# Kernel tuning notes

Measured on AMD Instinct MI355X. Metric: run time of the kernel, lower is better.

Reference implementation:

```python
import jax, jax.numpy as jnp
import numpy as np

UP_TIME = 1440.0
UP_DIST = 40.0
LOC_CNT = 100000
LOC_LEN = 131072
H = 256


def setup_inputs() -> dict:
    key = jax.random.key(0)
    ks = jax.random.split(key, 12)
    stdv = 1.0 / np.sqrt(H)
    u = lambda k, shape: jax.random.uniform(k, shape, jnp.float32, -stdv, stdv)
    return {
        "td_upper": jax.random.uniform(ks[0], (LOC_LEN,), jnp.float32),
        "td_lower": jax.random.uniform(ks[1], (LOC_LEN,), jnp.float32),
        "ld_upper": jax.random.uniform(ks[2], (LOC_LEN,), jnp.float32),
        "ld_lower": jax.random.uniform(ks[3], (LOC_LEN,), jnp.float32),
        "loc": jax.random.randint(ks[4], (LOC_LEN,), 0, LOC_CNT, jnp.int32),
        "hx": jax.random.normal(ks[5], (H, 1), jnp.float32),
        "weight_ih": u(ks[6], (H, H)),
        "weight_th_upper": u(ks[7], (H, H)),
        "weight_th_lower": u(ks[8], (H, H)),
        "weight_sh_upper": u(ks[9], (H, H)),
        "weight_sh_lower": u(ks[10], (H, H)),
        "location_weight": u(ks[11], (LOC_CNT, H)),
    }


def reference(td_upper, td_lower, ld_upper, ld_lower, loc, hx,
              weight_ih, weight_th_upper, weight_th_lower,
              weight_sh_upper, weight_sh_lower, location_weight):
    tu = jnp.clip(td_upper, 0.0, UP_TIME)
    tl = jnp.clip(td_lower, 0.0, UP_TIME)
    lu = jnp.clip(ld_upper, 0.0, UP_DIST)
    ll = jnp.clip(ld_lower, 0.0, UP_DIST)

    e = location_weight[loc]  # [L, H] gathered POI embeddings
    # Ttd[i] @ e[i] = (tu[i]*W_tu@e[i] + tl[i]*W_tl@e[i]) / (tu[i]+tl[i])
    a = jnp.einsum('hk,lk->lh', weight_th_upper, e)
    b = jnp.einsum('hk,lk->lh', weight_th_lower, e)
    t = (tu[:, None] * a + tl[:, None] * b) / (tu + tl)[:, None]  # [L, H]
    # Sld[i] @ t[i]
    c = jnp.einsum('hk,lk->lh', weight_sh_upper, t)
    d = jnp.einsum('hk,lk->lh', weight_sh_lower, t)
    s = (lu[:, None] * c + ll[:, None] * d) / (lu + ll)[:, None]  # [L, H]

    loc_vec = jnp.sum(s, axis=0)[:, None]  # [H, 1]
    usr_vec = weight_ih @ hx               # [H, 1]
    return jax.nn.sigmoid(loc_vec + usr_vec)
```

## Files before the change

### kernel.cpp

```cpp
#include <hip/hip_runtime.h>
#include <math.h>

#define H 256
#define TILE 256

__global__ __launch_bounds__(256) void strnn_gather(
    const float* __restrict__ td_u, const float* __restrict__ td_l,
    const float* __restrict__ ld_u, const float* __restrict__ ld_l,
    const int* __restrict__ loc, const float* __restrict__ table,
    float* __restrict__ v, int L)
{
    __shared__ float4 s_w[TILE];
    __shared__ int    s_loc[TILE];
    __shared__ float  s_red[4][4][H];
    const int t    = threadIdx.x;
    const int wave = t >> 6;
    const int lane = t & 63;

    float4 a0 = {0,0,0,0}, a1 = {0,0,0,0}, a2 = {0,0,0,0}, a3 = {0,0,0,0};

    for (int base = blockIdx.x * TILE; base < L; base += gridDim.x * TILE) {
        const int l = base + t;
        const bool ok = (l < L);
        float tu = ok ? fminf(fmaxf(td_u[l], 0.f), 1440.f) : 1.f;
        float tl = ok ? fminf(fmaxf(td_l[l], 0.f), 1440.f) : 1.f;
        float lu = ok ? fminf(fmaxf(ld_u[l], 0.f), 40.f)   : 1.f;
        float ll = ok ? fminf(fmaxf(ld_l[l], 0.f), 40.f)   : 1.f;
        float al = tu / (tu + tl);
        float be = lu / (lu + ll);
        float w0 = be * al, w1 = be * (1.f - al);
        float w2 = (1.f - be) * al, w3 = (1.f - be) * (1.f - al);
        if (!ok) { w0 = w1 = w2 = w3 = 0.f; }
        s_w[t]   = make_float4(w0, w1, w2, w3);
        s_loc[t] = ok ? loc[l] : 0;
        __syncthreads();

        const int r0 = wave * 64;
        #pragma unroll 2
        for (int j = 0; j < 64; j += 8) {
            const float4* addr[8];
            #pragma unroll
            for (int u = 0; u < 8; ++u)
                addr[u] = (const float4*)(table + (size_t)s_loc[r0 + j + u] * H + 4 * lane);
            float4 w[8], e[8];
            #pragma unroll
            for (int u = 0; u < 8; ++u)
                e[u] = *addr[u];
            #pragma unroll
            for (int u = 0; u < 8; ++u)
                w[u] = s_w[r0 + j + u];
            #pragma unroll
            for (int u = 0; u < 8; ++u) {
                a0.x = fmaf(w[u].x, e[u].x, a0.x);
                a0.y = fmaf(w[u].x, e[u].y, a0.y);
                a0.z = fmaf(w[u].x, e[u].z, a0.z);
                a0.w = fmaf(w[u].x, e[u].w, a0.w);
                a1.x = fmaf(w[u].y, e[u].x, a1.x);
                a1.y = fmaf(w[u].y, e[u].y, a1.y);
                a1.z = fmaf(w[u].y, e[u].z, a1.z);
                a1.w = fmaf(w[u].y, e[u].w, a1.w);
                a2.x = fmaf(w[u].z, e[u].x, a2.x);
                a2.y = fmaf(w[u].z, e[u].y, a2.y);
                a2.z = fmaf(w[u].z, e[u].z, a2.z);
                a2.w = fmaf(w[u].z, e[u].w, a2.w);
                a3.x = fmaf(w[u].w, e[u].x, a3.x);
                a3.y = fmaf(w[u].w, e[u].y, a3.y);
                a3.z = fmaf(w[u].w, e[u].z, a3.z);
                a3.w = fmaf(w[u].w, e[u].w, a3.w);
            }
        }
        __syncthreads();
    }

    *(float4*)&s_red[wave][0][4 * lane] = a0;
    *(float4*)&s_red[wave][1][4 * lane] = a1;
    *(float4*)&s_red[wave][2][4 * lane] = a2;
    *(float4*)&s_red[wave][3][4 * lane] = a3;
    __syncthreads();
    #pragma unroll
    for (int c = 0; c < 4; ++c) {
        float s = s_red[0][c][t] + s_red[1][c][t] + s_red[2][c][t] + s_red[3][c][t];
        atomicAdd(&v[c * H + t], s);
    }
}

__global__ __launch_bounds__(256) void strnn_mid(
    const float* __restrict__ Wtu, const float* __restrict__ Wtl,
    const float* __restrict__ Wih, const float* __restrict__ hx,
    const float* __restrict__ v, float* __restrict__ pqu)
{
    const int wave = (blockIdx.x * blockDim.x + threadIdx.x) >> 6;
    const int lane = threadIdx.x & 63;
    const float* v1 = v;
    const float* v2 = v + H;
    const float* v3 = v + 2 * H;
    const float* v4 = v + 3 * H;

    float p = 0.f, q = 0.f, u = 0.f;
    #pragma unroll
    for (int i = 0; i < H; i += 64) {
        const int k = i + lane;
        const float wtu = Wtu[wave * H + k];
        const float wtl = Wtl[wave * H + k];
        p = fmaf(wtu, v1[k], fmaf(wtl, v2[k], p));
        q = fmaf(wtu, v3[k], fmaf(wtl, v4[k], q));
        u = fmaf(Wih[wave * H + k], hx[k], u);
    }
    #pragma unroll
    for (int off = 32; off > 0; off >>= 1) {
        p += __shfl_down(p, off, 64);
        q += __shfl_down(q, off, 64);
        u += __shfl_down(u, off, 64);
    }
    if (lane == 0) {
        pqu[wave]         = p;
        pqu[H + wave]     = q;
        pqu[2 * H + wave] = u;
    }
}

__global__ __launch_bounds__(256) void strnn_out(
    const float* __restrict__ Wsu, const float* __restrict__ Wsl,
    const float* __restrict__ pqu, float* __restrict__ out)
{
    const int wave = (blockIdx.x * blockDim.x + threadIdx.x) >> 6;
    const int lane = threadIdx.x & 63;
    const float* p = pqu;
    const float* q = pqu + H;
    const float* u = pqu + 2 * H;

    float s = 0.f;
    #pragma unroll
    for (int i = 0; i < H; i += 64) {
        const int k = i + lane;
        s = fmaf(Wsu[wave * H + k], p[k], fmaf(Wsl[wave * H + k], q[k], s));
    }
    #pragma unroll
    for (int off = 32; off > 0; off >>= 1)
        s += __shfl_down(s, off, 64);
    if (lane == 0)
        out[wave] = 1.f / (1.f + expf(-(s + u[wave])));
}

extern "C" void kernel_launch(void* const* d_in, const int* in_sizes, int n_in,
                              void* d_out, int out_size, void* d_ws, size_t ws_size,
                              hipStream_t stream) {
    const float* td_u  = (const float*)d_in[0];
    const float* td_l  = (const float*)d_in[1];
    const float* ld_u  = (const float*)d_in[2];
    const float* ld_l  = (const float*)d_in[3];
    const int*   loc   = (const int*)d_in[4];
    const float* hx    = (const float*)d_in[5];
    const float* Wih   = (const float*)d_in[6];
    const float* Wtu   = (const float*)d_in[7];
    const float* Wtl   = (const float*)d_in[8];
    const float* Wsu   = (const float*)d_in[9];
    const float* Wsl   = (const float*)d_in[10];
    const float* table = (const float*)d_in[11];
    const int L = in_sizes[0];

    float* v   = (float*)d_ws;
    float* pqu = v + 4 * H;

    hipMemsetAsync(v, 0, 4 * H * sizeof(float), stream);

    strnn_gather<<<512, 256, 0, stream>>>(td_u, td_l, ld_u, ld_l, loc, table, v, L);
    strnn_mid<<<64, 256, 0, stream>>>(Wtu, Wtl, Wih, hx, v, pqu);
    strnn_out<<<64, 256, 0, stream>>>(Wsu, Wsl, pqu, (float*)d_out);
}
```

Measured before the change: 183.7 us.

## Aggregate weights per location by scatter, then stream embedding table once

Each sequence element's four mixing weights are now atomically added into a per-location weight buffer. A second kernel then streams the embedding table row by row, reading only rows with nonzero weight, and accumulates the weighted sums. This swaps random 1KB-per-element gathers, including repeated rows, for a mostly sequential pass over the table. The cost is global float atomics, a larger workspace memset and an extra kernel launch.

New measurement: 208.7 us. 1.14x slower.

```diff
diff --git a/kernel.cpp b/kernel.cpp
--- a/kernel.cpp
+++ b/kernel.cpp
@@ -2,74 +2,76 @@
 #include <math.h>
 
 #define H 256
-#define TILE 256
 
-__global__ __launch_bounds__(256) void strnn_gather(
+__global__ __launch_bounds__(256) void strnn_scatter(
     const float* __restrict__ td_u, const float* __restrict__ td_l,
     const float* __restrict__ ld_u, const float* __restrict__ ld_l,
-    const int* __restrict__ loc, const float* __restrict__ table,
-    float* __restrict__ v, int L)
+    const int* __restrict__ loc, float* __restrict__ W, int L)
 {
-    __shared__ float4 s_w[TILE];
-    __shared__ int    s_loc[TILE];
-    __shared__ float  s_red[4][4][H];
+    int i = blockIdx.x * blockDim.x + threadIdx.x;
+    const int stride = gridDim.x * blockDim.x;
+    for (; i < L; i += stride) {
+        const float tu = fminf(fmaxf(td_u[i], 0.f), 1440.f);
+        const float tl = fminf(fmaxf(td_l[i], 0.f), 1440.f);
+        const float lu = fminf(fmaxf(ld_u[i], 0.f), 40.f);
+        const float ll = fminf(fmaxf(ld_l[i], 0.f), 40.f);
+        const float al = tu / (tu + tl);
+        const float be = lu / (lu + ll);
+        float* Wr = W + 4 * (size_t)loc[i];
+        atomicAdd(Wr + 0, be * al);
+        atomicAdd(Wr + 1, be * (1.f - al));
+        atomicAdd(Wr + 2, (1.f - be) * al);
+        atomicAdd(Wr + 3, (1.f - be) * (1.f - al));
+    }
+}
+
+__global__ __launch_bounds__(512) void strnn_accum(
+    const float* __restrict__ W, const float* __restrict__ table,
+    float* __restrict__ v, int R)
+{
+    __shared__ float s_red[8][4][H];
     const int t    = threadIdx.x;
     const int wave = t >> 6;
     const int lane = t & 63;
+    const int nwave = gridDim.x * 8;
 
     float4 a0 = {0,0,0,0}, a1 = {0,0,0,0}, a2 = {0,0,0,0}, a3 = {0,0,0,0};
 
-    for (int base = blockIdx.x * TILE; base < L; base += gridDim.x * TILE) {
-        const int l = base + t;
-        const bool ok = (l < L);
-        float tu = ok ? fminf(fmaxf(td_u[l], 0.f), 1440.f) : 1.f;
-        float tl = ok ? fminf(fmaxf(td_l[l], 0.f), 1440.f) : 1.f;
-        float lu = ok ? fminf(fmaxf(ld_u[l], 0.f), 40.f)   : 1.f;
-        float ll = ok ? fminf(fmaxf(ld_l[l], 0.f), 40.f)   : 1.f;
-        float al = tu / (tu + tl);
-        float be = lu / (lu + ll);
-        float w0 = be * al, w1 = be * (1.f - al);
-        float w2 = (1.f - be) * al, w3 = (1.f - be) * (1.f - al);
-        if (!ok) { w0 = w1 = w2 = w3 = 0.f; }
-        s_w[t]   = make_float4(w0, w1, w2, w3);
-        s_loc[t] = ok ? loc[l] : 0;
-        __syncthreads();
-
-        const int r0 = wave * 64;
-        #pragma unroll 2
-        for (int j = 0; j < 64; j += 8) {
-            const float4* addr[8];
-            #pragma unroll
-            for (int u = 0; u < 8; ++u)
-                addr[u] = (const float4*)(table + (size_t)s_loc[r0 + j + u] * H + 4 * lane);
-            float4 w[8], e[8];
-            #pragma unroll
-            for (int u = 0; u < 8; ++u)
-                e[u] = *addr[u];
-            #pragma unroll
-            for (int u = 0; u < 8; ++u)
-                w[u] = s_w[r0 + j + u];
-            #pragma unroll
-            for (int u = 0; u < 8; ++u) {
-                a0.x = fmaf(w[u].x, e[u].x, a0.x);
-                a0.y = fmaf(w[u].x, e[u].y, a0.y);
-                a0.z = fmaf(w[u].x, e[u].z, a0.z);
-                a0.w = fmaf(w[u].x, e[u].w, a0.w);
-                a1.x = fmaf(w[u].y, e[u].x, a1.x);
-                a1.y = fmaf(w[u].y, e[u].y, a1.y);
-                a1.z = fmaf(w[u].y, e[u].z, a1.z);
-                a1.w = fmaf(w[u].y, e[u].w, a1.w);
-                a2.x = fmaf(w[u].z, e[u].x, a2.x);
-                a2.y = fmaf(w[u].z, e[u].y, a2.y);
-                a2.z = fmaf(w[u].z, e[u].z, a2.z);
-                a2.w = fmaf(w[u].z, e[u].w, a2.w);
-                a3.x = fmaf(w[u].w, e[u].x, a3.x);
-                a3.y = fmaf(w[u].w, e[u].y, a3.y);
-                a3.z = fmaf(w[u].w, e[u].z, a3.z);
-                a3.w = fmaf(w[u].w, e[u].w, a3.w);
-            }
+    for (int r0 = (blockIdx.x * 8 + wave) * 8; r0 < R; r0 += nwave * 8) {
+        float4 wv[8], e[8];
+        #pragma unroll
+        for (int u = 0; u < 8; ++u) {
+            const int r = r0 + u;
+            wv[u] = (r < R) ? *(const float4*)(W + 4 * (size_t)r)
+                            : make_float4(0.f, 0.f, 0.f, 0.f);
         }
-        __syncthreads();
+        #pragma unroll
+        for (int u = 0; u < 8; ++u) {
+            e[u] = make_float4(0.f, 0.f, 0.f, 0.f);
+            const float4 w = wv[u];
+            if (w.x != 0.f || w.y != 0.f || w.z != 0.f || w.w != 0.f)
+                e[u] = *(const float4*)(table + (size_t)(r0 + u) * H + 4 * lane);
+        }
+        #pragma unroll
+        for (int u = 0; u < 8; ++u) {
+            const float4 w = wv[u];
+            a0.x = fmaf(w.x, e[u].x, a0.x);
+            a0.y = fmaf(w.x, e[u].y, a0.y);
+            a0.z = fmaf(w.x, e[u].z, a0.z);
+            a0.w = fmaf(w.x, e[u].w, a0.w);
+            a1.x = fmaf(w.y, e[u].x, a1.x);
+            a1.y = fmaf(w.y, e[u].y, a1.y);
+            a1.z = fmaf(w.y, e[u].z, a1.z);
+            a1.w = fmaf(w.y, e[u].w, a1.w);
+            a2.x = fmaf(w.z, e[u].x, a2.x);
+            a2.y = fmaf(w.z, e[u].y, a2.y);
+            a2.z = fmaf(w.z, e[u].z, a2.z);
+            a2.w = fmaf(w.z, e[u].w, a2.w);
+            a3.x = fmaf(w.w, e[u].x, a3.x);
+            a3.y = fmaf(w.w, e[u].y, a3.y);
+            a3.z = fmaf(w.w, e[u].z, a3.z);
+            a3.w = fmaf(w.w, e[u].w, a3.w);
+        }
     }
 
     *(float4*)&s_red[wave][0][4 * lane] = a0;
@@ -77,10 +79,15 @@
     *(float4*)&s_red[wave][2][4 * lane] = a2;
     *(float4*)&s_red[wave][3][4 * lane] = a3;
     __syncthreads();
+    const int col = t & 255;
     #pragma unroll
-    for (int c = 0; c < 4; ++c) {
-        float s = s_red[0][c][t] + s_red[1][c][t] + s_red[2][c][t] + s_red[3][c][t];
-        atomicAdd(&v[c * H + t], s);
+    for (int cc = 0; cc < 2; ++cc) {
+        const int c = (t >> 8) * 2 + cc;
+        float s = 0.f;
+        #pragma unroll
+        for (int wv_ = 0; wv_ < 8; ++wv_)
+            s += s_red[wv_][c][col];
+        atomicAdd(&v[c * H + col], s);
     }
 }
 
@@ -158,13 +165,16 @@
     const float* Wsl   = (const float*)d_in[10];
     const float* table = (const float*)d_in[11];
     const int L = in_sizes[0];
+    const int R = in_sizes[11] / H;
 
-    float* v   = (float*)d_ws;
+    float* W   = (float*)d_ws;
+    float* v   = W + (size_t)R * 4;
     float* pqu = v + 4 * H;
 
-    hipMemsetAsync(v, 0, 4 * H * sizeof(float), stream);
+    hipMemsetAsync(W, 0, ((size_t)R * 4 + 4 * H) * sizeof(float), stream);
 
-    strnn_gather<<<512, 256, 0, stream>>>(td_u, td_l, ld_u, ld_l, loc, table, v, L);
+    strnn_scatter<<<512, 256, 0, stream>>>(td_u, td_l, ld_u, ld_l, loc, W, L);
+    strnn_accum<<<512, 512, 0, stream>>>(W, table, v, R);
     strnn_mid<<<64, 256, 0, stream>>>(Wtu, Wtl, Wih, hx, v, pqu);
     strnn_out<<<64, 256, 0, stream>>>(Wsu, Wsl, pqu, (float*)d_out);
 }
```

## Replace atomics and memset with per-block partials and fused mid/out kernel

Applied to the files above, without the earlier changes.

The gather kernel now writes per-block partial sums to workspace instead of doing global atomicAdds, which also removes the memset launch. A single fused kernel of 64 blocks reduces the partials, then runs the mid and output matvecs, separated by grid-wide spin barriers built on counters. The intent is to cut launch overhead and atomic contention. In exchange it relies on all 64 blocks being co-resident for the spin barriers, and adds a partials buffer that must be written and read back.

Measured after the change: 189.5 us. 1.03x slower.

```diff
diff --git a/kernel.cpp b/kernel.cpp
--- a/kernel.cpp
+++ b/kernel.cpp
@@ -3,12 +3,15 @@
 
 #define H 256
 #define TILE 256
+#define NBLK 512
+#define NMID 64
+
 
 __global__ __launch_bounds__(256) void strnn_gather(
     const float* __restrict__ td_u, const float* __restrict__ td_l,
     const float* __restrict__ ld_u, const float* __restrict__ ld_l,
     const int* __restrict__ loc, const float* __restrict__ table,
-    float* __restrict__ v, int L)
+    unsigned* __restrict__ hdr, float* __restrict__ part, int L)
 {
     __shared__ float4 s_w[TILE];
     __shared__ int    s_loc[TILE];
@@ -16,6 +19,8 @@
     const int t    = threadIdx.x;
     const int wave = t >> 6;
     const int lane = t & 63;
+
+    if (blockIdx.x == 0 && t < 64) hdr[t] = 0u;
 
     float4 a0 = {0,0,0,0}, a1 = {0,0,0,0}, a2 = {0,0,0,0}, a3 = {0,0,0,0};
 
@@ -77,69 +82,116 @@
     *(float4*)&s_red[wave][2][4 * lane] = a2;
     *(float4*)&s_red[wave][3][4 * lane] = a3;
     __syncthreads();
+    float* pb = part + (size_t)blockIdx.x * 4 * H;
     #pragma unroll
     for (int c = 0; c < 4; ++c) {
         float s = s_red[0][c][t] + s_red[1][c][t] + s_red[2][c][t] + s_red[3][c][t];
-        atomicAdd(&v[c * H + t], s);
+        pb[c * H + t] = s;
     }
 }
 
-__global__ __launch_bounds__(256) void strnn_mid(
+__global__ __launch_bounds__(256) void strnn_midout(
     const float* __restrict__ Wtu, const float* __restrict__ Wtl,
-    const float* __restrict__ Wih, const float* __restrict__ hx,
-    const float* __restrict__ v, float* __restrict__ pqu)
+    const float* __restrict__ Wih, const float* __restrict__ Wsu,
+    const float* __restrict__ Wsl, const float* __restrict__ hx,
+    const float* __restrict__ part, float* __restrict__ v,
+    float* __restrict__ pqu, unsigned* __restrict__ hdr,
+    float* __restrict__ out)
 {
-    const int wave = (blockIdx.x * blockDim.x + threadIdx.x) >> 6;
-    const int lane = threadIdx.x & 63;
-    const float* v1 = v;
-    const float* v2 = v + H;
-    const float* v3 = v + 2 * H;
-    const float* v4 = v + 3 * H;
-
-    float p = 0.f, q = 0.f, u = 0.f;
-    #pragma unroll
-    for (int i = 0; i < H; i += 64) {
-        const int k = i + lane;
-        const float wtu = Wtu[wave * H + k];
-        const float wtl = Wtl[wave * H + k];
-        p = fmaf(wtu, v1[k], fmaf(wtl, v2[k], p));
-        q = fmaf(wtu, v3[k], fmaf(wtl, v4[k], q));
-        u = fmaf(Wih[wave * H + k], hx[k], u);
-    }
-    #pragma unroll
-    for (int off = 32; off > 0; off >>= 1) {
-        p += __shfl_down(p, off, 64);
-        q += __shfl_down(q, off, 64);
-        u += __shfl_down(u, off, 64);
-    }
-    if (lane == 0) {
-        pqu[wave]         = p;
-        pqu[H + wave]     = q;
-        pqu[2 * H + wave] = u;
-    }
-}
-
-__global__ __launch_bounds__(256) void strnn_out(
-    const float* __restrict__ Wsu, const float* __restrict__ Wsl,
-    const float* __restrict__ pqu, float* __restrict__ out)
-{
-    const int wave = (blockIdx.x * blockDim.x + threadIdx.x) >> 6;
-    const int lane = threadIdx.x & 63;
-    const float* p = pqu;
-    const float* q = pqu + H;
-    const float* u = pqu + 2 * H;
-
-    float s = 0.f;
-    #pragma unroll
-    for (int i = 0; i < H; i += 64) {
-        const int k = i + lane;
-        s = fmaf(Wsu[wave * H + k], p[k], fmaf(Wsl[wave * H + k], q[k], s));
-    }
-    #pragma unroll
-    for (int off = 32; off > 0; off >>= 1)
-        s += __shfl_down(s, off, 64);
-    if (lane == 0)
-        out[wave] = 1.f / (1.f + expf(-(s + u[wave])));
+    __shared__ float s_red[16][17];
+    const int j    = blockIdx.x;
+    const int t    = threadIdx.x;
+    const int wave = t >> 6;
+    const int lane = t & 63;
+
+    {
+        const int c  = j >> 4;
+        const int h0 = (j & 15) * 16;
+        const int hh = t & 15;
+        const int b0 = t >> 4;
+        float s = 0.f;
+        #pragma unroll 8
+        for (int b = b0; b < NBLK; b += 16)
+            s += part[((size_t)b * 4 + c) * H + h0 + hh];
+        s_red[b0][hh] = s;
+        __syncthreads();
+        if (t < 16) {
+            float acc = 0.f;
+            #pragma unroll
+            for (int k = 0; k < 16; ++k) acc += s_red[k][t];
+            __hip_atomic_store(&v[c * H + h0 + t], acc,
+                               __ATOMIC_RELAXED, __HIP_MEMORY_SCOPE_AGENT);
+        }
+    }
+    __threadfence();
+    __syncthreads();
+    if (t == 0)
+        __hip_atomic_fetch_add(&hdr[0], 1u,
+                               __ATOMIC_RELEASE, __HIP_MEMORY_SCOPE_AGENT);
+    if (t == 0) {
+        while (__hip_atomic_load(&hdr[0], __ATOMIC_ACQUIRE,
+                                 __HIP_MEMORY_SCOPE_AGENT) < NMID)
+            __builtin_amdgcn_s_sleep(1);
+    }
+    __syncthreads();
+
+    const int h = j * 4 + wave;
+    {
+        float p = 0.f, q = 0.f, u = 0.f;
+        #pragma unroll
+        for (int i = 0; i < H; i += 64) {
+            const int k = i + lane;
+            const float v1 = __hip_atomic_load(&v[k],         __ATOMIC_RELAXED, __HIP_MEMORY_SCOPE_AGENT);
+            const float v2 = __hip_atomic_load(&v[H + k],     __ATOMIC_RELAXED, __HIP_MEMORY_SCOPE_AGENT);
+            const float v3 = __hip_atomic_load(&v[2 * H + k], __ATOMIC_RELAXED, __HIP_MEMORY_SCOPE_AGENT);
+            const float v4 = __hip_atomic_load(&v[3 * H + k], __ATOMIC_RELAXED, __HIP_MEMORY_SCOPE_AGENT);
+            const float wtu = Wtu[h * H + k];
+            const float wtl = Wtl[h * H + k];
+            p = fmaf(wtu, v1, fmaf(wtl, v2, p));
+            q = fmaf(wtu, v3, fmaf(wtl, v4, q));
+            u = fmaf(Wih[h * H + k], hx[k], u);
+        }
+        #pragma unroll
+        for (int off = 32; off > 0; off >>= 1) {
+            p += __shfl_down(p, off, 64);
+            q += __shfl_down(q, off, 64);
+            u += __shfl_down(u, off, 64);
+        }
+        if (lane == 0) {
+            __hip_atomic_store(&pqu[h],         p, __ATOMIC_RELAXED, __HIP_MEMORY_SCOPE_AGENT);
+            __hip_atomic_store(&pqu[H + h],     q, __ATOMIC_RELAXED, __HIP_MEMORY_SCOPE_AGENT);
+            __hip_atomic_store(&pqu[2 * H + h], u, __ATOMIC_RELAXED, __HIP_MEMORY_SCOPE_AGENT);
+        }
+    }
+    __threadfence();
+    __syncthreads();
+    if (t == 0)
+        __hip_atomic_fetch_add(&hdr[32], 1u,
+                               __ATOMIC_RELEASE, __HIP_MEMORY_SCOPE_AGENT);
+    if (t == 0) {
+        while (__hip_atomic_load(&hdr[32], __ATOMIC_ACQUIRE,
+                                 __HIP_MEMORY_SCOPE_AGENT) < NMID)
+            __builtin_amdgcn_s_sleep(1);
+    }
+    __syncthreads();
+
+    {
+        float s = 0.f;
+        #pragma unroll
+        for (int i = 0; i < H; i += 64) {
+            const int k = i + lane;
+            const float pk = __hip_atomic_load(&pqu[k],     __ATOMIC_RELAXED, __HIP_MEMORY_SCOPE_AGENT);
+            const float qk = __hip_atomic_load(&pqu[H + k], __ATOMIC_RELAXED, __HIP_MEMORY_SCOPE_AGENT);
+            s = fmaf(Wsu[h * H + k], pk, fmaf(Wsl[h * H + k], qk, s));
+        }
+        #pragma unroll
+        for (int off = 32; off > 0; off >>= 1)
+            s += __shfl_down(s, off, 64);
+        if (lane == 0) {
+            const float u = __hip_atomic_load(&pqu[2 * H + h], __ATOMIC_RELAXED, __HIP_MEMORY_SCOPE_AGENT);
+            out[h] = 1.f / (1.f + expf(-(s + u)));
+        }
+    }
 }
 
 extern "C" void kernel_launch(void* const* d_in, const int* in_sizes, int n_in,
@@ -159,12 +211,14 @@
     const float* table = (const float*)d_in[11];
     const int L = in_sizes[0];
 
-    float* v   = (float*)d_ws;
-    float* pqu = v + 4 * H;
-
-    hipMemsetAsync(v, 0, 4 * H * sizeof(float), stream);
-
-    strnn_gather<<<512, 256, 0, stream>>>(td_u, td_l, ld_u, ld_l, loc, table, v, L);
-    strnn_mid<<<64, 256, 0, stream>>>(Wtu, Wtl, Wih, hx, v, pqu);
-    strnn_out<<<64, 256, 0, stream>>>(Wsu, Wsl, pqu, (float*)d_out);
+    float*    ws   = (float*)d_ws;
+    unsigned* hdr  = (unsigned*)ws;
+    float*    v    = ws + 64;
+    float*    pqu  = ws + 64 + 4 * H;
+    float*    part = ws + 2048;
+
+    strnn_gather<<<NBLK, 256, 0, stream>>>(
+        td_u, td_l, ld_u, ld_l, loc, table, hdr, part, L);
+    strnn_midout<<<NMID, 256, 0, stream>>>(
+        Wtu, Wtl, Wih, Wsu, Wsl, hx, part, v, pqu, hdr, (float*)d_out);
 }
```

## Bucket gather events by location row range before embedding gather

Applied to the files above, without the earlier changes.

Adds a bucketize kernel that histograms loc values into 512 buckets of 256 rows, computes a global prefix sum through a grid-wide spin barrier, and scatters the precomputed weights and loc indices into bucket order. The gather kernel then reads embedding rows in roughly sorted order, so rows that are close in memory are fetched together and cache and TLB locality should improve. The cost is an extra pass over the inputs, global atomics for the scatter, and a software grid barrier that assumes all 256 blocks are resident at the same time. The float accumulation order also changes.

New measurement: 278.5 us. +51.6%, slower.

```diff
diff --git a/kernel.cpp b/kernel.cpp
--- a/kernel.cpp
+++ b/kernel.cpp
@@ -3,12 +3,95 @@
 
 #define H 256
 #define TILE 256
-
-__global__ __launch_bounds__(256) void strnn_gather(
+#define NBLK 512
+#define NABC 256
+#define NBKT 512
+
+
+typedef unsigned u32;
+
+__global__ __launch_bounds__(256) void strnn_bucketize(
     const float* __restrict__ td_u, const float* __restrict__ td_l,
     const float* __restrict__ ld_u, const float* __restrict__ ld_l,
-    const int* __restrict__ loc, const float* __restrict__ table,
-    float* __restrict__ v, int L)
+    const int* __restrict__ loc, u32* __restrict__ hdr, int* __restrict__ cur,
+    int* __restrict__ ev_loc, float4* __restrict__ ev_w, int L)
+{
+    __shared__ int s_h[NBKT];
+    const int t = threadIdx.x;
+
+    #pragma unroll
+    for (int i = t; i < NBKT; i += 256) s_h[i] = 0;
+    __syncthreads();
+    for (int i = blockIdx.x * 256 + t; i < L; i += NABC * 256)
+        atomicAdd(&s_h[((u32)loc[i]) >> 8], 1);
+    __syncthreads();
+    #pragma unroll
+    for (int i = t; i < NBKT; i += 256) {
+        const int c = s_h[i];
+        if (c) atomicAdd(&cur[i], c);
+    }
+
+    __threadfence();
+    __syncthreads();
+    if (t == 0)
+        __hip_atomic_fetch_add(&hdr[0], 1u, __ATOMIC_RELEASE,
+                               __HIP_MEMORY_SCOPE_AGENT);
+    if (blockIdx.x == 0) {
+        if (t == 0)
+            while (__hip_atomic_load(&hdr[0], __ATOMIC_ACQUIRE,
+                                     __HIP_MEMORY_SCOPE_AGENT) < NABC)
+                __builtin_amdgcn_s_sleep(1);
+        __syncthreads();
+
+        #pragma unroll
+        for (int i = t; i < NBKT; i += 256)
+            s_h[i] = __hip_atomic_load(&cur[i], __ATOMIC_RELAXED,
+                                       __HIP_MEMORY_SCOPE_AGENT);
+        __syncthreads();
+        for (int off = 1; off < NBKT; off <<= 1) {
+            const int i0 = t, i1 = t + 256;
+            const int a0 = (i0 >= off) ? s_h[i0 - off] : 0;
+            const int a1 = (i1 >= off) ? s_h[i1 - off] : 0;
+            __syncthreads();
+            s_h[i0] += a0;
+            s_h[i1] += a1;
+            __syncthreads();
+        }
+        #pragma unroll
+        for (int i = t; i < NBKT; i += 256)
+            __hip_atomic_store(&cur[i], i ? s_h[i - 1] : 0, __ATOMIC_RELAXED,
+                               __HIP_MEMORY_SCOPE_AGENT);
+        __threadfence();
+        __syncthreads();
+        if (t == 0)
+            __hip_atomic_store(&hdr[32], 1u, __ATOMIC_RELEASE,
+                               __HIP_MEMORY_SCOPE_AGENT);
+    } else {
+        if (t == 0)
+            while (__hip_atomic_load(&hdr[32], __ATOMIC_ACQUIRE,
+                                     __HIP_MEMORY_SCOPE_AGENT) == 0)
+                __builtin_amdgcn_s_sleep(1);
+    }
+    __syncthreads();
+
+    for (int i = blockIdx.x * 256 + t; i < L; i += NABC * 256) {
+        const float tu = fminf(fmaxf(td_u[i], 0.f), 1440.f);
+        const float tl = fminf(fmaxf(td_l[i], 0.f), 1440.f);
+        const float lu = fminf(fmaxf(ld_u[i], 0.f), 40.f);
+        const float ll = fminf(fmaxf(ld_l[i], 0.f), 40.f);
+        const float al = tu / (tu + tl);
+        const float be = lu / (lu + ll);
+        const int r = loc[i];
+        const int pos = atomicAdd(&cur[((u32)r) >> 8], 1);
+        ev_loc[pos] = r;
+        ev_w[pos] = make_float4(be * al, be * (1.f - al),
+                                (1.f - be) * al, (1.f - be) * (1.f - al));
+    }
+}
+
+__global__ __launch_bounds__(256) void strnn_gather(
+    const int* __restrict__ ev_loc, const float4* __restrict__ ev_w,
+    const float* __restrict__ table, float* __restrict__ v, int L)
 {
     __shared__ float4 s_w[TILE];
     __shared__ int    s_loc[TILE];
@@ -22,17 +105,8 @@
     for (int base = blockIdx.x * TILE; base < L; base += gridDim.x * TILE) {
         const int l = base + t;
         const bool ok = (l < L);
-        float tu = ok ? fminf(fmaxf(td_u[l], 0.f), 1440.f) : 1.f;
-        float tl = ok ? fminf(fmaxf(td_l[l], 0.f), 1440.f) : 1.f;
-        float lu = ok ? fminf(fmaxf(ld_u[l], 0.f), 40.f)   : 1.f;
-        float ll = ok ? fminf(fmaxf(ld_l[l], 0.f), 40.f)   : 1.f;
-        float al = tu / (tu + tl);
-        float be = lu / (lu + ll);
-        float w0 = be * al, w1 = be * (1.f - al);
-        float w2 = (1.f - be) * al, w3 = (1.f - be) * (1.f - al);
-        if (!ok) { w0 = w1 = w2 = w3 = 0.f; }
-        s_w[t]   = make_float4(w0, w1, w2, w3);
-        s_loc[t] = ok ? loc[l] : 0;
+        s_w[t]   = ok ? ev_w[l] : make_float4(0.f, 0.f, 0.f, 0.f);
+        s_loc[t] = ok ? ev_loc[l] : 0;
         __syncthreads();
 
         const int r0 = wave * 64;
@@ -159,12 +233,19 @@
     const float* table = (const float*)d_in[11];
     const int L = in_sizes[0];
 
-    float* v   = (float*)d_ws;
-    float* pqu = v + 4 * H;
-
-    hipMemsetAsync(v, 0, 4 * H * sizeof(float), stream);
-
-    strnn_gather<<<512, 256, 0, stream>>>(td_u, td_l, ld_u, ld_l, loc, table, v, L);
+    float*  ws     = (float*)d_ws;
+    u32*    hdr    = (u32*)ws;
+    int*    cur    = (int*)(ws + 64);
+    float*  v      = ws + 576;
+    float*  pqu    = ws + 1600;
+    int*    ev_loc = (int*)(ws + 4096);
+    float4* ev_w   = (float4*)(ws + 4096 + L);
+
+    hipMemsetAsync(ws, 0, 6400, stream);
+
+    strnn_bucketize<<<NABC, 256, 0, stream>>>(
+        td_u, td_l, ld_u, ld_l, loc, hdr, cur, ev_loc, ev_w, L);
+    strnn_gather<<<NBLK, 256, 0, stream>>>(ev_loc, ev_w, table, v, L);
     strnn_mid<<<64, 256, 0, stream>>>(Wtu, Wtl, Wih, hx, v, pqu);
     strnn_out<<<64, 256, 0, stream>>>(Wsu, Wsl, pqu, (float*)d_out);
 }
```
